# Kernel tuning notes

Hardware: AMD Instinct MI355X
Metric: run time of the kernel (lower is better)

The kernel has to match this reference:

```python
import jax, jax.numpy as jnp
import numpy as np

B, IN, C, H, E = 8192, 768, 64, 64, 16  # batch, input_dim, n_concepts, hidden_dim, embedding_dim


def setup_inputs() -> dict:
    key = jax.random.key(0)
    ks = jax.random.split(key, 10)

    def w(k, shape, fan_in):
        return jax.random.normal(k, shape, jnp.float32) / np.float32(np.sqrt(fan_in))

    inp = {"x": jax.random.normal(ks[0], (B, IN), jnp.float32)}
    i = 1
    for pre, din, dout in (("pos", IN, E), ("neg", IN, E), ("cp", 2 * E, 1)):
        inp[pre + "_W1"] = w(ks[i], (C, din, H), din)
        inp[pre + "_b1"] = jnp.zeros((C, H), jnp.float32)
        inp[pre + "_W2"] = w(ks[i + 1], (C, H, H), H)
        inp[pre + "_b2"] = jnp.zeros((C, H), jnp.float32)
        inp[pre + "_W3"] = w(ks[i + 2], (C, H, dout), H)
        inp[pre + "_b3"] = jnp.zeros((C, dout), jnp.float32)
        i += 3
    return inp


def _bank(x, W1, b1, W2, b2, W3, b3):
    # x: [B, IN]; per-concept MLP batched over C via einsum -> [B, C, E]
    h = jax.nn.relu(jnp.einsum('bi,cih->bch', x, W1) + b1)
    h = jax.nn.relu(jnp.einsum('bch,cho->bco', h, W2) + b2)
    return jnp.einsum('bch,che->bce', h, W3) + b3


def reference(x, pos_W1, pos_b1, pos_W2, pos_b2, pos_W3, pos_b3,
              neg_W1, neg_b1, neg_W2, neg_b2, neg_W3, neg_b3,
              cp_W1, cp_b1, cp_W2, cp_b2, cp_W3, cp_b3):
    pos = _bank(x, pos_W1, pos_b1, pos_W2, pos_b2, pos_W3, pos_b3)  # [B,C,E]
    neg = _bank(x, neg_W1, neg_b1, neg_W2, neg_b2, neg_W3, neg_b3)  # [B,C,E]
    # torch cat([pos, neg], dim=1) on [B,E,C], then x[:,:,i] -> per-concept [B, 2E]
    xc = jnp.concatenate([pos, neg], axis=-1)  # [B,C,2E]
    h = jax.nn.relu(jnp.einsum('bci,cih->bch', xc, cp_W1) + cp_b1)
    h = jax.nn.relu(jnp.einsum('bch,cho->bco', h, cp_W2) + cp_b2)
    concepts = (jnp.einsum('bch,cho->bco', h, cp_W3) + cp_b3)[..., 0]  # [B,C]
    w = jnp.clip(concepts * 0.5 + 0.5, 0.0, 1.0)[:, :, None]  # gate in [0,1]
    emb = pos * w + neg * (1.0 - w)  # [B,C,E]
    # torch layout is [B,E,C] then .view(B,-1): transpose before flattening
    emb_flat = jnp.transpose(emb, (0, 2, 1)).reshape(x.shape[0], E * C)
    return emb_flat, concepts
```

## Files before the change

### kernel.cpp

```cpp
#include <hip/hip_runtime.h>
#include <hip/hip_bf16.h>


#define B_   8192
#define IN_  768
#define C_   64
#define H_   64
#define E_   16
#define BM_  128

typedef __bf16 bf16x8 __attribute__((ext_vector_type(8)));
typedef float  f32x4  __attribute__((ext_vector_type(4)));

__device__ __forceinline__ f32x4 mfma16(bf16x8 a, bf16x8 b, f32x4 c) {
  return __builtin_amdgcn_mfma_f32_16x16x32_bf16(a, b, c, 0, 0, 0);
}

__device__ __forceinline__ bf16x8 cvt8(float4 a, float4 b) {
  bf16x8 r;
  r[0] = (__bf16)a.x; r[1] = (__bf16)a.y; r[2] = (__bf16)a.z; r[3] = (__bf16)a.w;
  r[4] = (__bf16)b.x; r[5] = (__bf16)b.y; r[6] = (__bf16)b.z; r[7] = (__bf16)b.w;
  return r;
}

__device__ __forceinline__ void zero_acc(f32x4 (&acc)[2][4]) {
  const f32x4 z = {0.f, 0.f, 0.f, 0.f};
#pragma unroll
  for (int mt = 0; mt < 2; ++mt)
#pragma unroll
    for (int nt = 0; nt < 4; ++nt) acc[mt][nt] = z;
}

struct __align__(16) SmemT {
  __bf16 xs[BM_ * 72];
  __bf16 wt[64 * 72];
  __bf16 xcb[BM_ * 40];
  float  conc[BM_];
};
static_assert(sizeof(SmemT) <= 40960, "LDS overflow");

__device__ __forceinline__ void epi72(__bf16* __restrict__ hb, f32x4 (&acc)[2][4],
                                      const float* __restrict__ bias,
                                      int wave, int quad, int l16) {
#pragma unroll
  for (int nt = 0; nt < 4; ++nt) {
    const int col = nt * 16 + l16;
    const float bv = bias[col];
#pragma unroll
    for (int mt = 0; mt < 2; ++mt)
#pragma unroll
      for (int r = 0; r < 4; ++r) {
        int row = wave * 32 + mt * 16 + quad * 4 + r;
        hb[row * 72 + col] = (__bf16)fmaxf(acc[mt][nt][r] + bv, 0.f);
      }
  }
}

__device__ __forceinline__ void gemm64(const __bf16* __restrict__ hb,
                                       const __bf16* __restrict__ wt,
                                       f32x4 (&acc)[2][4], int wave, int quad, int l16) {
#pragma unroll
  for (int ks = 0; ks < 2; ++ks) {
    bf16x8 a[2], bb[4];
#pragma unroll
    for (int mt = 0; mt < 2; ++mt)
      a[mt] = *(const bf16x8*)(hb + (wave * 32 + mt * 16 + l16) * 72 + ks * 32 + quad * 8);
#pragma unroll
    for (int nt = 0; nt < 4; ++nt)
      bb[nt] = *(const bf16x8*)(wt + (nt * 16 + l16) * 72 + ks * 32 + quad * 8);
#pragma unroll
    for (int mt = 0; mt < 2; ++mt)
#pragma unroll
      for (int nt = 0; nt < 4; ++nt)
        acc[mt][nt] = mfma16(a[mt], bb[nt], acc[mt][nt]);
  }
}

__device__ __forceinline__ void stage_w64(const __bf16* __restrict__ Wt,
                                          __bf16* __restrict__ wt, int tid) {
#pragma unroll
  for (int it = 0; it < 2; ++it) {
    int q = tid + it * 256;
    int n = q >> 3, i = q & 7;
    *(uint4*)&wt[n * 72 + i * 8] = *(const uint4*)(Wt + n * 64 + i * 8);
  }
}

__device__ __forceinline__ void run_bank_t(SmemT& sm, const __bf16* __restrict__ x,
    const __bf16* __restrict__ W1t, const float* __restrict__ b1,
    const __bf16* __restrict__ W2t, const float* __restrict__ b2,
    const __bf16* __restrict__ W3t, const float* __restrict__ b3,
    int row0, int xc_off, int tid, int wave, int quad, int l16)
{
  __bf16* xs = sm.xs;
  __bf16* wt = sm.wt;
  __bf16* hb = sm.xs;

  f32x4 acc1[2][4]; zero_acc(acc1);
  const int sr = tid >> 3, si = tid & 7;
  const __bf16* xg = x + (size_t)row0 * IN_;
  for (int kt = 0; kt < IN_ / 64; ++kt) {
    const int ko = kt * 64;
    uint4 xv[4], wv[2];
#pragma unroll
    for (int it = 0; it < 4; ++it)
      xv[it] = *(const uint4*)(xg + (size_t)(sr + it * 32) * IN_ + ko + si * 8);
#pragma unroll
    for (int it = 0; it < 2; ++it)
      wv[it] = *(const uint4*)(W1t + (size_t)(sr + it * 32) * IN_ + ko + si * 8);
#pragma unroll
    for (int it = 0; it < 4; ++it)
      *(uint4*)&xs[(sr + it * 32) * 72 + si * 8] = xv[it];
#pragma unroll
    for (int it = 0; it < 2; ++it)
      *(uint4*)&wt[(sr + it * 32) * 72 + si * 8] = wv[it];
    __syncthreads();
#pragma unroll
    for (int ks = 0; ks < 2; ++ks) {
      bf16x8 a[2], bb[4];
#pragma unroll
      for (int mt = 0; mt < 2; ++mt)
        a[mt] = *(const bf16x8*)&xs[(wave * 32 + mt * 16 + l16) * 72 + ks * 32 + quad * 8];
#pragma unroll
      for (int nt = 0; nt < 4; ++nt)
        bb[nt] = *(const bf16x8*)&wt[(nt * 16 + l16) * 72 + ks * 32 + quad * 8];
#pragma unroll
      for (int mt = 0; mt < 2; ++mt)
#pragma unroll
        for (int nt = 0; nt < 4; ++nt)
          acc1[mt][nt] = mfma16(a[mt], bb[nt], acc1[mt][nt]);
    }
    __syncthreads();
  }
  epi72(hb, acc1, b1, wave, quad, l16);
  stage_w64(W2t, wt, tid);
  __syncthreads();

  f32x4 acc2[2][4]; zero_acc(acc2);
  gemm64(hb, wt, acc2, wave, quad, l16);
  __syncthreads();
  epi72(hb, acc2, b2, wave, quad, l16);
  if (tid < 128)
    *(uint4*)&wt[(tid >> 3) * 72 + (tid & 7) * 8] =
        *(const uint4*)(W3t + (tid >> 3) * 64 + (tid & 7) * 8);
  __syncthreads();

  f32x4 acc3[2];
  { const f32x4 z = {0.f, 0.f, 0.f, 0.f}; acc3[0] = z; acc3[1] = z; }
#pragma unroll
  for (int ks = 0; ks < 2; ++ks) {
    bf16x8 bb = *(const bf16x8*)&wt[l16 * 72 + ks * 32 + quad * 8];
#pragma unroll
    for (int mt = 0; mt < 2; ++mt) {
      bf16x8 a = *(const bf16x8*)&hb[(wave * 32 + mt * 16 + l16) * 72 + ks * 32 + quad * 8];
      acc3[mt] = mfma16(a, bb, acc3[mt]);
    }
  }
  {
    float bv = b3[l16];
#pragma unroll
    for (int mt = 0; mt < 2; ++mt)
#pragma unroll
      for (int r = 0; r < 4; ++r) {
        int row = wave * 32 + mt * 16 + quad * 4 + r;
        sm.xcb[row * 40 + xc_off + l16] = (__bf16)(acc3[mt][r] + bv);
      }
  }
  __syncthreads();
}

__global__ __launch_bounds__(256, 4) void cb_fused_t(
    const __bf16* __restrict__ x,
    const __bf16* __restrict__ pW1t, const float* __restrict__ pb1,
    const __bf16* __restrict__ pW2t, const float* __restrict__ pb2,
    const __bf16* __restrict__ pW3t, const float* __restrict__ pb3,
    const __bf16* __restrict__ nW1t, const float* __restrict__ nb1,
    const __bf16* __restrict__ nW2t, const float* __restrict__ nb2,
    const __bf16* __restrict__ nW3t, const float* __restrict__ nb3,
    const __bf16* __restrict__ cW1t, const float* __restrict__ cb1,
    const __bf16* __restrict__ cW2t, const float* __restrict__ cb2,
    const __bf16* __restrict__ cw3,  const float* __restrict__ cb3,
    float* __restrict__ out_emb, float* __restrict__ out_con)
{
  __shared__ SmemT sm;
  const int tid  = threadIdx.x;
  const int wave = tid >> 6, lane = tid & 63;
  const int quad = lane >> 4, l16 = lane & 15;
  const int row0 = blockIdx.x * BM_;
  const int c    = blockIdx.y;
  __bf16* hb = sm.xs;
  __bf16* wt = sm.wt;

  run_bank_t(sm, x, pW1t + (size_t)c * 64 * IN_, pb1 + c * 64,
             pW2t + (size_t)c * 64 * 64, pb2 + c * 64,
             pW3t + (size_t)c * 16 * 64, pb3 + c * 16,
             row0, 0, tid, wave, quad, l16);
  run_bank_t(sm, x, nW1t + (size_t)c * 64 * IN_, nb1 + c * 64,
             nW2t + (size_t)c * 64 * 64, nb2 + c * 64,
             nW3t + (size_t)c * 16 * 64, nb3 + c * 16,
             row0, 16, tid, wave, quad, l16);

  {
    int n = tid >> 2, i = tid & 3;
    *(uint4*)&wt[n * 72 + i * 8] = *(const uint4*)(cW1t + ((size_t)c * 64 + n) * 32 + i * 8);
  }
  __syncthreads();
  f32x4 acc1[2][4]; zero_acc(acc1);
  {
    bf16x8 a[2], bb[4];
#pragma unroll
    for (int mt = 0; mt < 2; ++mt)
      a[mt] = *(const bf16x8*)&sm.xcb[(wave * 32 + mt * 16 + l16) * 40 + quad * 8];
#pragma unroll
    for (int nt = 0; nt < 4; ++nt)
      bb[nt] = *(const bf16x8*)&wt[(nt * 16 + l16) * 72 + quad * 8];
#pragma unroll
    for (int mt = 0; mt < 2; ++mt)
#pragma unroll
      for (int nt = 0; nt < 4; ++nt)
        acc1[mt][nt] = mfma16(a[mt], bb[nt], acc1[mt][nt]);
  }
  __syncthreads();
  epi72(hb, acc1, cb1 + c * 64, wave, quad, l16);
  stage_w64(cW2t + (size_t)c * 64 * 64, wt, tid);
  __syncthreads();

  f32x4 acc2[2][4]; zero_acc(acc2);
  gemm64(hb, wt, acc2, wave, quad, l16);
  __syncthreads();
  epi72(hb, acc2, cb2 + c * 64, wave, quad, l16);
  if (tid < 8) *(uint4*)&wt[tid * 8] = *(const uint4*)(cw3 + (size_t)c * 64 + tid * 8);
  __syncthreads();

  f32x4 acc3[2];
  { const f32x4 z = {0.f, 0.f, 0.f, 0.f}; acc3[0] = z; acc3[1] = z; }
#pragma unroll
  for (int ks = 0; ks < 2; ++ks) {
    bf16x8 bb = {};
    if (l16 == 0) bb = *(const bf16x8*)&wt[ks * 32 + quad * 8];
#pragma unroll
    for (int mt = 0; mt < 2; ++mt) {
      bf16x8 a = *(const bf16x8*)&hb[(wave * 32 + mt * 16 + l16) * 72 + ks * 32 + quad * 8];
      acc3[mt] = mfma16(a, bb, acc3[mt]);
    }
  }
  if (l16 == 0) {
    float bv = cb3[c];
#pragma unroll
    for (int mt = 0; mt < 2; ++mt)
#pragma unroll
      for (int r = 0; r < 4; ++r)
        sm.conc[wave * 32 + mt * 16 + quad * 4 + r] = acc3[mt][r] + bv;
  }
  __syncthreads();

  for (int ii = tid; ii < BM_ * E_; ii += 256) {
    int row = ii >> 4, e = ii & 15;
    float cv = sm.conc[row];
    float w  = fminf(fmaxf(cv * 0.5f + 0.5f, 0.f), 1.f);
    float pv2 = (float)sm.xcb[row * 40 + e];
    float nv2 = (float)sm.xcb[row * 40 + 16 + e];
    out_emb[(size_t)(row0 + row) * (E_ * C_) + e * C_ + c] = pv2 * w + nv2 * (1.f - w);
  }
  if (tid < 128) out_con[(size_t)(row0 + tid) * C_ + c] = sm.conc[tid];
}

#define TSEG 5
#define PSEG 5
struct PrepArgs {
  const float* tsrc[TSEG];
  __bf16*      tdst[TSEG];
  int tstart[TSEG + 1];
  int ktiles[TSEG];
  const float* psrc[PSEG];
  __bf16*      pdst[PSEG];
  int pstart[PSEG + 1];
  int pchunks[PSEG];
  int kdiv8[PSEG];
  int N[PSEG];
  int tblocks;
};

__global__ __launch_bounds__(256) void prep_all(PrepArgs a) {
  const int tid = threadIdx.x;
  const int b = blockIdx.x;
  __shared__ __bf16 lt[64 * 72];
  if (b < a.tblocks) {
    int s = 0;
    while (s < TSEG - 1 && b >= a.tstart[s + 1]) ++s;
    const int idx = b - a.tstart[s];
    const int kt = idx % a.ktiles[s];
    const int c  = idx / a.ktiles[s];
    const int K  = a.ktiles[s] * 64;
    const float* src = a.tsrc[s] + (size_t)c * K * 64 + (size_t)kt * 64 * 64;
    __bf16*      dst = a.tdst[s] + (size_t)c * 64 * K + kt * 64;
    const int r = tid >> 4, c4 = (tid & 15) * 4;
#pragma unroll
    for (int it = 0; it < 4; ++it) {
      int k = r + it * 16;
      float4 v = *(const float4*)(src + (size_t)k * 64 + c4);
      lt[(c4 + 0) * 72 + k] = (__bf16)v.x;
      lt[(c4 + 1) * 72 + k] = (__bf16)v.y;
      lt[(c4 + 2) * 72 + k] = (__bf16)v.z;
      lt[(c4 + 3) * 72 + k] = (__bf16)v.w;
    }
    __syncthreads();
    const int n = tid >> 3, i = tid & 7;
#pragma unroll
    for (int it = 0; it < 2; ++it) {
      int nn = n + it * 32;
      *(uint4*)(dst + (size_t)nn * K + i * 8) = *(const uint4*)&lt[nn * 72 + i * 8];
    }
  } else {
    const int bb = b - a.tblocks;
    int s = 0;
    while (s < PSEG - 1 && bb >= a.pstart[s + 1]) ++s;
    const int lb  = bb - a.pstart[s];
    const int nch = a.pchunks[s];
    const int kc  = a.kdiv8[s];
    const int N   = a.N[s];
#pragma unroll
    for (int j = 0; j < 4; ++j) {
      const int li = (lb * 4 + j) * 256 + tid;
      if (li >= nch) break;
      if (N == 1) {
        const float4* src = (const float4*)a.psrc[s] + (size_t)li * 2;
        float4 v0 = src[0], v1 = src[1];
        *(uint4*)(a.pdst[s] + (size_t)li * 8) = __builtin_bit_cast(uint4, cvt8(v0, v1));
      } else {
        int rn = li / kc;
        int k0 = (li - rn * kc) * 8;
        int cc = rn / N;
        int n  = rn - cc * N;
        const float* src = a.psrc[s] + ((size_t)cc * kc * 8 + k0) * N + n;
        bf16x8 r;
#pragma unroll
        for (int jj = 0; jj < 8; ++jj) r[jj] = (__bf16)src[(size_t)jj * N];
        *(uint4*)(a.pdst[s] + (size_t)rn * kc * 8 + k0) = __builtin_bit_cast(uint4, r);
      }
    }
  }
}

extern "C" void kernel_launch(void* const* d_in, const int* in_sizes, int n_in,
                              void* d_out, int out_size, void* d_ws, size_t ws_size,
                              hipStream_t stream) {
  const float* xf   = (const float*)d_in[0];
  const float* pW1f = (const float*)d_in[1];
  const float* pb1f = (const float*)d_in[2];
  const float* pW2f = (const float*)d_in[3];
  const float* pb2f = (const float*)d_in[4];
  const float* pW3f = (const float*)d_in[5];
  const float* pb3f = (const float*)d_in[6];
  const float* nW1f = (const float*)d_in[7];
  const float* nb1f = (const float*)d_in[8];
  const float* nW2f = (const float*)d_in[9];
  const float* nb2f = (const float*)d_in[10];
  const float* nW3f = (const float*)d_in[11];
  const float* nb3f = (const float*)d_in[12];
  const float* cW1f = (const float*)d_in[13];
  const float* cb1f = (const float*)d_in[14];
  const float* cW2f = (const float*)d_in[15];
  const float* cb2f = (const float*)d_in[16];
  const float* cW3f = (const float*)d_in[17];
  const float* cb3f = (const float*)d_in[18];

  float* out_emb = (float*)d_out;
  float* out_con = out_emb + (size_t)B_ * E_ * C_;

  const int cx   = B_ * IN_;
  const int cW1c = C_ * IN_ * H_;
  const int cW2c = C_ * H_ * H_;
  const int cW3c = C_ * H_ * E_;
  const int ccW1 = C_ * 2 * E_ * H_;
  const int ccW3 = C_ * H_;

  __bf16* w = (__bf16*)d_ws;
  size_t o = 0;
  __bf16* xw   = w + o; o += cx;
  __bf16* pw1t = w + o; o += cW1c;
  __bf16* nw1t = w + o; o += cW1c;
  __bf16* pw2t = w + o; o += cW2c;
  __bf16* nw2t = w + o; o += cW2c;
  __bf16* cw2t = w + o; o += cW2c;
  __bf16* pw3t = w + o; o += cW3c;
  __bf16* nw3t = w + o; o += cW3c;
  __bf16* cw1t = w + o; o += ccW1;
  __bf16* cw3w = w + o; o += ccW3;

  PrepArgs a;
  int tb = 0, pb = 0;
  {
    const float* tsrc[TSEG] = {pW1f, nW1f, pW2f, nW2f, cW2f};
    __bf16*      tdst[TSEG] = {pw1t, nw1t, pw2t, nw2t, cw2t};
    const int    tk[TSEG]   = {12,   12,   1,    1,    1};
    for (int i = 0; i < TSEG; ++i) {
      a.tsrc[i] = tsrc[i]; a.tdst[i] = tdst[i]; a.ktiles[i] = tk[i];
      a.tstart[i] = tb;
      tb += tk[i] * C_;
    }
    a.tstart[TSEG] = tb;
    a.tblocks = tb;

    const float* psrc[PSEG] = {xf, cW3f, pW3f, nW3f, cW1f};
    __bf16*      pdst[PSEG] = {xw, cw3w, pw3t, nw3t, cw1t};
    const int    pKs[PSEG]  = {0,  0,    64,   64,   32};
    const int    pNs[PSEG]  = {1,  1,    16,   16,   64};
    const int    pels[PSEG] = {cx, ccW3, cW3c, cW3c, ccW1};
    for (int i = 0; i < PSEG; ++i) {
      a.psrc[i] = psrc[i]; a.pdst[i] = pdst[i];
      a.pchunks[i] = pels[i] / 8;
      a.kdiv8[i] = (pNs[i] == 1) ? (pels[i] / 8) : (pKs[i] / 8);
      a.N[i] = pNs[i];
      a.pstart[i] = pb;
      pb += (pels[i] / 8 + 1023) / 1024;
    }
    a.pstart[PSEG] = pb;
  }
  prep_all<<<tb + pb, 256, 0, stream>>>(a);

  dim3 grid(B_ / BM_, C_);
  cb_fused_t<<<grid, 256, 0, stream>>>(xw,
      pw1t, pb1f, pw2t, pb2f, pw3t, pb3f,
      nw1t, nb1f, nw2t, nb2f, nw3t, nb3f,
      cw1t, cb1f, cw2t, cb2f, cw3w, cb3f,
      out_emb, out_con);
}
```

Before: 336.5 us.

## Fuse pos and neg bank layer-1 GEMMs to share each staged x tile

The pos and neg first-layer GEMMs now run in a single K loop, so each x tile is read from global memory and written to LDS once instead of twice. Both banks' W1 tiles sit side by side in a doubled weight buffer. Layers 2 and 3 for the two banks are interleaved to reuse the hb buffer. In exchange LDS grows to about 47 KB, accumulator registers double, and launch bounds drop from 4 to 3 blocks per CU, which lowers occupancy.

```diff
diff --git a/kernel.cpp b/kernel.cpp
--- a/kernel.cpp
+++ b/kernel.cpp
@@ -33,11 +33,12 @@
 
 struct __align__(16) SmemT {
   __bf16 xs[BM_ * 72];
-  __bf16 wt[64 * 72];
+  __bf16 wt[128 * 72];
   __bf16 xcb[BM_ * 40];
   float  conc[BM_];
 };
-static_assert(sizeof(SmemT) <= 40960, "LDS overflow");
+static_assert(sizeof(SmemT) == 47616, "layout");
+static_assert(sizeof(SmemT) <= 54613, "LDS: need 3 blocks/CU");
 
 __device__ __forceinline__ void epi72(__bf16* __restrict__ hb, f32x4 (&acc)[2][4],
                                       const float* __restrict__ bias,
@@ -86,90 +87,33 @@
   }
 }
 
-__device__ __forceinline__ void run_bank_t(SmemT& sm, const __bf16* __restrict__ x,
-    const __bf16* __restrict__ W1t, const float* __restrict__ b1,
-    const __bf16* __restrict__ W2t, const float* __restrict__ b2,
-    const __bf16* __restrict__ W3t, const float* __restrict__ b3,
-    int row0, int xc_off, int tid, int wave, int quad, int l16)
-{
-  __bf16* xs = sm.xs;
-  __bf16* wt = sm.wt;
-  __bf16* hb = sm.xs;
-
-  f32x4 acc1[2][4]; zero_acc(acc1);
-  const int sr = tid >> 3, si = tid & 7;
-  const __bf16* xg = x + (size_t)row0 * IN_;
-  for (int kt = 0; kt < IN_ / 64; ++kt) {
-    const int ko = kt * 64;
-    uint4 xv[4], wv[2];
-#pragma unroll
-    for (int it = 0; it < 4; ++it)
-      xv[it] = *(const uint4*)(xg + (size_t)(sr + it * 32) * IN_ + ko + si * 8);
-#pragma unroll
-    for (int it = 0; it < 2; ++it)
-      wv[it] = *(const uint4*)(W1t + (size_t)(sr + it * 32) * IN_ + ko + si * 8);
-#pragma unroll
-    for (int it = 0; it < 4; ++it)
-      *(uint4*)&xs[(sr + it * 32) * 72 + si * 8] = xv[it];
-#pragma unroll
-    for (int it = 0; it < 2; ++it)
-      *(uint4*)&wt[(sr + it * 32) * 72 + si * 8] = wv[it];
-    __syncthreads();
-#pragma unroll
-    for (int ks = 0; ks < 2; ++ks) {
-      bf16x8 a[2], bb[4];
-#pragma unroll
-      for (int mt = 0; mt < 2; ++mt)
-        a[mt] = *(const bf16x8*)&xs[(wave * 32 + mt * 16 + l16) * 72 + ks * 32 + quad * 8];
-#pragma unroll
-      for (int nt = 0; nt < 4; ++nt)
-        bb[nt] = *(const bf16x8*)&wt[(nt * 16 + l16) * 72 + ks * 32 + quad * 8];
-#pragma unroll
-      for (int mt = 0; mt < 2; ++mt)
-#pragma unroll
-        for (int nt = 0; nt < 4; ++nt)
-          acc1[mt][nt] = mfma16(a[mt], bb[nt], acc1[mt][nt]);
-    }
-    __syncthreads();
-  }
-  epi72(hb, acc1, b1, wave, quad, l16);
-  stage_w64(W2t, wt, tid);
-  __syncthreads();
-
-  f32x4 acc2[2][4]; zero_acc(acc2);
-  gemm64(hb, wt, acc2, wave, quad, l16);
-  __syncthreads();
-  epi72(hb, acc2, b2, wave, quad, l16);
-  if (tid < 128)
-    *(uint4*)&wt[(tid >> 3) * 72 + (tid & 7) * 8] =
-        *(const uint4*)(W3t + (tid >> 3) * 64 + (tid & 7) * 8);
-  __syncthreads();
-
+__device__ __forceinline__ void l3_tile(const __bf16* __restrict__ hb,
+                                        const __bf16* __restrict__ wt16,
+                                        __bf16* __restrict__ xcb,
+                                        const float* __restrict__ b3, int xc_off,
+                                        int wave, int quad, int l16) {
   f32x4 acc3[2];
   { const f32x4 z = {0.f, 0.f, 0.f, 0.f}; acc3[0] = z; acc3[1] = z; }
 #pragma unroll
   for (int ks = 0; ks < 2; ++ks) {
-    bf16x8 bb = *(const bf16x8*)&wt[l16 * 72 + ks * 32 + quad * 8];
+    bf16x8 bb = *(const bf16x8*)(wt16 + l16 * 72 + ks * 32 + quad * 8);
 #pragma unroll
     for (int mt = 0; mt < 2; ++mt) {
-      bf16x8 a = *(const bf16x8*)&hb[(wave * 32 + mt * 16 + l16) * 72 + ks * 32 + quad * 8];
+      bf16x8 a = *(const bf16x8*)(hb + (wave * 32 + mt * 16 + l16) * 72 + ks * 32 + quad * 8);
       acc3[mt] = mfma16(a, bb, acc3[mt]);
     }
   }
-  {
-    float bv = b3[l16];
-#pragma unroll
-    for (int mt = 0; mt < 2; ++mt)
-#pragma unroll
-      for (int r = 0; r < 4; ++r) {
-        int row = wave * 32 + mt * 16 + quad * 4 + r;
-        sm.xcb[row * 40 + xc_off + l16] = (__bf16)(acc3[mt][r] + bv);
-      }
-  }
-  __syncthreads();
-}
-
-__global__ __launch_bounds__(256, 4) void cb_fused_t(
+  const float bv = b3[l16];
+#pragma unroll
+  for (int mt = 0; mt < 2; ++mt)
+#pragma unroll
+    for (int r = 0; r < 4; ++r) {
+      int row = wave * 32 + mt * 16 + quad * 4 + r;
+      xcb[row * 40 + xc_off + l16] = (__bf16)(acc3[mt][r] + bv);
+    }
+}
+
+__global__ __launch_bounds__(256, 3) void cb_fused_t(
     const __bf16* __restrict__ x,
     const __bf16* __restrict__ pW1t, const float* __restrict__ pb1,
     const __bf16* __restrict__ pW2t, const float* __restrict__ pb2,
@@ -188,17 +132,95 @@
   const int quad = lane >> 4, l16 = lane & 15;
   const int row0 = blockIdx.x * BM_;
   const int c    = blockIdx.y;
+  __bf16* xs = sm.xs;
+  __bf16* wt = sm.wt;
   __bf16* hb = sm.xs;
-  __bf16* wt = sm.wt;
-
-  run_bank_t(sm, x, pW1t + (size_t)c * 64 * IN_, pb1 + c * 64,
-             pW2t + (size_t)c * 64 * 64, pb2 + c * 64,
-             pW3t + (size_t)c * 16 * 64, pb3 + c * 16,
-             row0, 0, tid, wave, quad, l16);
-  run_bank_t(sm, x, nW1t + (size_t)c * 64 * IN_, nb1 + c * 64,
-             nW2t + (size_t)c * 64 * 64, nb2 + c * 64,
-             nW3t + (size_t)c * 16 * 64, nb3 + c * 16,
-             row0, 16, tid, wave, quad, l16);
+
+  const __bf16* pg   = pW1t + (size_t)c * 64 * IN_;
+  const __bf16* ng   = nW1t + (size_t)c * 64 * IN_;
+  const float*  pb1c = pb1 + c * 64;
+  const float*  nb1c = nb1 + c * 64;
+  const float*  pb2c = pb2 + c * 64;
+  const float*  nb2c = nb2 + c * 64;
+
+  f32x4 accP[2][4]; zero_acc(accP);
+  f32x4 accN[2][4]; zero_acc(accN);
+  const int sr = tid >> 3, si = tid & 7;
+  const __bf16* xg = x + (size_t)row0 * IN_;
+  for (int kt = 0; kt < IN_ / 64; ++kt) {
+    const int ko = kt * 64;
+    uint4 xv[4], pv[2], nv[2];
+#pragma unroll
+    for (int it = 0; it < 4; ++it)
+      xv[it] = *(const uint4*)(xg + (size_t)(sr + it * 32) * IN_ + ko + si * 8);
+#pragma unroll
+    for (int it = 0; it < 2; ++it) {
+      pv[it] = *(const uint4*)(pg + (size_t)(sr + it * 32) * IN_ + ko + si * 8);
+      nv[it] = *(const uint4*)(ng + (size_t)(sr + it * 32) * IN_ + ko + si * 8);
+    }
+#pragma unroll
+    for (int it = 0; it < 4; ++it)
+      *(uint4*)&xs[(sr + it * 32) * 72 + si * 8] = xv[it];
+#pragma unroll
+    for (int it = 0; it < 2; ++it) {
+      *(uint4*)&wt[(sr + it * 32) * 72 + si * 8]        = pv[it];
+      *(uint4*)&wt[(64 + sr + it * 32) * 72 + si * 8]   = nv[it];
+    }
+    __syncthreads();
+#pragma unroll
+    for (int ks = 0; ks < 2; ++ks) {
+      bf16x8 a[2], bp[4], bn[4];
+#pragma unroll
+      for (int mt = 0; mt < 2; ++mt)
+        a[mt] = *(const bf16x8*)&xs[(wave * 32 + mt * 16 + l16) * 72 + ks * 32 + quad * 8];
+#pragma unroll
+      for (int nt = 0; nt < 4; ++nt) {
+        bp[nt] = *(const bf16x8*)&wt[(nt * 16 + l16) * 72 + ks * 32 + quad * 8];
+        bn[nt] = *(const bf16x8*)&wt[(64 + nt * 16 + l16) * 72 + ks * 32 + quad * 8];
+      }
+#pragma unroll
+      for (int mt = 0; mt < 2; ++mt)
+#pragma unroll
+        for (int nt = 0; nt < 4; ++nt) {
+          accP[mt][nt] = mfma16(a[mt], bp[nt], accP[mt][nt]);
+          accN[mt][nt] = mfma16(a[mt], bn[nt], accN[mt][nt]);
+        }
+    }
+    __syncthreads();
+  }
+
+  epi72(hb, accP, pb1c, wave, quad, l16);
+  stage_w64(pW2t + (size_t)c * 64 * 64, wt, tid);
+  stage_w64(nW2t + (size_t)c * 64 * 64, wt + 64 * 72, tid);
+  __syncthreads();
+
+  f32x4 acc2P[2][4]; zero_acc(acc2P);
+  gemm64(hb, wt, acc2P, wave, quad, l16);
+  __syncthreads();
+
+  epi72(hb, accN, nb1c, wave, quad, l16);
+  {
+    int n = tid >> 3, i = tid & 7;
+    const __bf16* src = (n < 16)
+        ? (pW3t + (size_t)c * 16 * 64 + n * 64 + i * 8)
+        : (nW3t + (size_t)c * 16 * 64 + (n - 16) * 64 + i * 8);
+    *(uint4*)&wt[n * 72 + i * 8] = *(const uint4*)src;
+  }
+  __syncthreads();
+
+  f32x4 acc2N[2][4]; zero_acc(acc2N);
+  gemm64(hb, wt + 64 * 72, acc2N, wave, quad, l16);
+  __syncthreads();
+
+  epi72(hb, acc2P, pb2c, wave, quad, l16);
+  __syncthreads();
+  l3_tile(hb, wt, sm.xcb, pb3 + c * 16, 0, wave, quad, l16);
+  __syncthreads();
+
+  epi72(hb, acc2N, nb2c, wave, quad, l16);
+  __syncthreads();
+  l3_tile(hb, wt + 16 * 72, sm.xcb, nb3 + c * 16, 16, wave, quad, l16);
+  __syncthreads();
 
   {
     int n = tid >> 2, i = tid & 3;
```

New measurement: 311.9 us. -7.3%, faster.
